# Kernel optimization log

Hardware: AMD Instinct MI355X
Metric: run time of the kernel (lower is better)

Reference implementation:

```python
import jax, jax.numpy as jnp
import numpy as np

N = 100000
IN_F, C1, C2, C3, OUT_F = 64, 64, 64, 64, 8


def setup_inputs() -> dict:
    key = jax.random.key(0)
    ks = jax.random.split(key, 12)
    x = jax.random.normal(ks[0], (N, IN_F), dtype=jnp.float32)
    edge_index = jax.random.randint(ks[1], (2, 1600000), 0, N, dtype=jnp.int64)

    def lin(kw, kb, fi, fo):
        s = 1.0 / np.sqrt(fi)
        W = jax.random.uniform(kw, (fi, fo), jnp.float32, -s, s)
        b = jax.random.uniform(kb, (fo,), jnp.float32, -s, s)
        return W, b

    W1, b1 = lin(ks[2], ks[3], IN_F, C1)
    W2, b2 = lin(ks[4], ks[5], C1, C2)
    W3, b3 = lin(ks[6], ks[7], C2, C3)
    Wl, bl = lin(ks[8], ks[9], C3, OUT_F)
    return {"x": x, "edge_index": edge_index, "W1": W1, "b1": b1,
            "W2": W2, "b2": b2, "W3": W3, "b3": b3, "Wl": Wl, "bl": bl}


def _gcn_norm(edge_index, n):
    # add self loops, compute symmetric normalization D^-1/2 A D^-1/2
    loops = jnp.arange(n, dtype=edge_index.dtype)
    src = jnp.concatenate([edge_index[0], loops])
    dst = jnp.concatenate([edge_index[1], loops])
    deg = jax.ops.segment_sum(jnp.ones_like(dst, dtype=jnp.float32), dst, num_segments=n)
    dis = jnp.where(deg > 0, jax.lax.rsqrt(deg), 0.0)
    norm = dis[src] * dis[dst]  # [E+N]
    return src, dst, norm


def _gcn_layer(h, W, b, src, dst, norm, n):
    h = h @ W                                   # [N, Fout] small GEMM
    msg = h[src] * norm[:, None]                # gather + scale, [E+N, Fout]
    agg = jax.ops.segment_sum(msg, dst, num_segments=n)  # scatter-add
    return agg + b


def reference(x, edge_index, W1, b1, W2, b2, W3, b3, Wl, bl):
    n = x.shape[0]
    src, dst, norm = _gcn_norm(edge_index, n)
    h = jax.nn.relu(_gcn_layer(x, W1, b1, src, dst, norm, n))
    h = jax.nn.relu(_gcn_layer(h, W2, b2, src, dst, norm, n))
    h = jax.nn.relu(_gcn_layer(h, W3, b3, src, dst, norm, n))
    return h @ Wl + bl
```

## Files before the change

### kernel.cpp

```cpp
#include <hip/hip_runtime.h>
#include <hip/hip_fp16.h>

#define F 64
#define CHUNK 2048
#define BN 512
#define BSHIFT 9
#define CAP 20480

typedef int v4i __attribute__((ext_vector_type(4)));
typedef float fx4 __attribute__((ext_vector_type(4)));
typedef float v2f __attribute__((ext_vector_type(2)));
typedef _Float16 h8f __attribute__((ext_vector_type(8)));

union FB8 { uint4 u; h8f h; };
union FX4P { fx4 v; v2f p[2]; };

__global__ __launch_bounds__(256) void k_blkcnt(const int* __restrict__ dst,
                                                int* __restrict__ blkcnt,
                                                int E, int NB, int NBKT) {
    __shared__ int lcnt[256];
    int b = blockIdx.x, t = threadIdx.x;
    lcnt[t] = 0;
    __syncthreads();
    const v4i* d4 = (const v4i*)dst;
    int g0 = (b * CHUNK) >> 2;
    int E4 = E >> 2;
#pragma unroll
    for (int k = 0; k < 2; ++k) {
        int gi = g0 + k * 256 + t;
        if (gi < E4) {
            v4i q = __builtin_nontemporal_load(d4 + gi);
            atomicAdd(&lcnt[q.x >> BSHIFT], 1);
            atomicAdd(&lcnt[q.y >> BSHIFT], 1);
            atomicAdd(&lcnt[q.z >> BSHIFT], 1);
            atomicAdd(&lcnt[q.w >> BSHIFT], 1);
        }
    }
    __syncthreads();
    if (t < NBKT) blkcnt[t * NB + b] = lcnt[t];
}

__global__ __launch_bounds__(256) void k_bktscan(const int* __restrict__ blkcnt,
                                                 int* __restrict__ blkoff,
                                                 int* __restrict__ bkttot, int NB) {
    __shared__ int s[256];
    __shared__ int running;
    int seg = blockIdx.x;
    int t = threadIdx.x;
    if (t == 0) running = 0;
    __syncthreads();
    for (int base = 0; base < NB; base += 256) {
        int i = base + t;
        int v = (i < NB) ? blkcnt[seg * NB + i] : 0;
        s[t] = v;
        __syncthreads();
        for (int off = 1; off < 256; off <<= 1) {
            int x = (t >= off) ? s[t - off] : 0;
            __syncthreads();
            s[t] += x;
            __syncthreads();
        }
        int rbase = running;
        if (i < NB) blkoff[seg * NB + i] = rbase + s[t] - v;
        int ctot = s[255];
        __syncthreads();
        if (t == 0) running = rbase + ctot;
        __syncthreads();
    }
    if (t == 0) bkttot[seg] = running;
}

__global__ void k_sb(const int* __restrict__ bkttot, int* __restrict__ sb, int NBKT) {
    __shared__ int s[256];
    int t = threadIdx.x;
    int v = (t < NBKT) ? bkttot[t] : 0;
    s[t] = v;
    __syncthreads();
    for (int off = 1; off < 256; off <<= 1) {
        int x = (t >= off) ? s[t - off] : 0;
        __syncthreads();
        s[t] += x;
        __syncthreads();
    }
    if (t < NBKT) sb[t] = s[t] - v;
    if (t == NBKT - 1) sb[NBKT] = s[t];
}

__global__ __launch_bounds__(256) void k_stage2(const int* __restrict__ src,
                                                const int* __restrict__ dst,
                                                const int* __restrict__ blkoff,
                                                const int* __restrict__ sb,
                                                unsigned* __restrict__ stage,
                                                int E, int NB, int NBKT) {
    __shared__ int lcnt[256];
    __shared__ int lbase[257];
    __shared__ int obase[256];
    __shared__ int s[256];
    __shared__ unsigned rec[CHUNK];
    __shared__ unsigned char binof[CHUNK];
    int b = blockIdx.x, t = threadIdx.x;
    lcnt[t] = 0;
    __syncthreads();
    const v4i* d4 = (const v4i*)dst;
    const v4i* s4 = (const v4i*)src;
    int g0 = (b * CHUNK) >> 2;
    int E4 = E >> 2;
    int myseg[8], myrank[8];
    unsigned myrec[8];
#pragma unroll
    for (int k = 0; k < 2; ++k) {
        int gi = g0 + k * 256 + t;
        bool ok = gi < E4;
        v4i qd = {0, 0, 0, 0}, qs = {0, 0, 0, 0};
        if (ok) {
            qd = __builtin_nontemporal_load(d4 + gi);
            qs = __builtin_nontemporal_load(s4 + gi);
        }
        int dd[4] = {qd.x, qd.y, qd.z, qd.w};
        int ss[4] = {qs.x, qs.y, qs.z, qs.w};
#pragma unroll
        for (int j = 0; j < 4; ++j) {
            int idx = k * 4 + j;
            myseg[idx] = -1;
            if (ok) {
                int sg = dd[j] >> BSHIFT;
                myseg[idx] = sg;
                myrank[idx] = atomicAdd(&lcnt[sg], 1);
                myrec[idx] = ((unsigned)(dd[j] & (BN - 1)) << 17) | (unsigned)ss[j];
            }
        }
    }
    __syncthreads();
    int v = lcnt[t];
    s[t] = v;
    __syncthreads();
    for (int off = 1; off < 256; off <<= 1) {
        int x = (t >= off) ? s[t - off] : 0;
        __syncthreads();
        s[t] += x;
        __syncthreads();
    }
    lbase[t] = s[t] - v;
    if (t == 255) lbase[256] = s[255];
    obase[t] = (t < NBKT) ? sb[t] + blkoff[t * NB + b] : 0;
    __syncthreads();
#pragma unroll
    for (int k = 0; k < 8; ++k) {
        if (myseg[k] >= 0) {
            int p = lbase[myseg[k]] + myrank[k];
            rec[p] = myrec[k];
            binof[p] = (unsigned char)myseg[k];
        }
    }
    __syncthreads();
    int tot = lbase[256];
    for (int j = t; j < tot; j += 256) {
        int sg = binof[j];
        stage[obase[sg] + (j - lbase[sg])] = rec[j];
    }
}

__global__ __launch_bounds__(1024) void k_bincount(const unsigned* __restrict__ stage,
                                                   const int* __restrict__ sb,
                                                   int* __restrict__ count,
                                                   float* __restrict__ dis,
                                                   int* __restrict__ padtot, int n) {
    __shared__ int lc[BN];
    int bkt = blockIdx.x, t = threadIdx.x;
    int nb0 = bkt << BSHIFT;
    if (t < BN) lc[t] = 0;
    __syncthreads();
    int r0 = sb[bkt], r1 = sb[bkt + 1];
    for (int j = r0 + t; j < r1; j += 1024) {
        unsigned r = stage[j];
        atomicAdd(&lc[r >> 17], 1);
    }
    __syncthreads();
    int pv = 0;
    if (t < BN) {
        int node = nb0 + t;
        int cv = lc[t];
        if (node < n) {
            count[node] = cv;
            dis[node] = rsqrtf((float)(cv + 1));
            pv = (cv + 3) & ~3;
        }
    }
    __syncthreads();
    if (t < BN) lc[t] = pv;
    __syncthreads();
    for (int off = 256; off > 0; off >>= 1) {
        if (t < off) lc[t] += lc[t + off];
        __syncthreads();
    }
    if (t == 0) padtot[bkt] = lc[0];
}

__global__ void k_sb2(const int* __restrict__ padtot, int* __restrict__ rbase,
                      int* __restrict__ row_start, int NBKT, int n) {
    __shared__ int s[256];
    int t = threadIdx.x;
    int v = (t < NBKT) ? padtot[t] : 0;
    s[t] = v;
    __syncthreads();
    for (int off = 1; off < 256; off <<= 1) {
        int x = (t >= off) ? s[t - off] : 0;
        __syncthreads();
        s[t] += x;
        __syncthreads();
    }
    if (t < NBKT) rbase[t] = s[t] - v;
    if (t == NBKT - 1) { rbase[NBKT] = s[t]; row_start[n] = s[t]; }
}

__global__ __launch_bounds__(512) void k_binfill(const unsigned* __restrict__ stage,
                                                 const int* __restrict__ sb,
                                                 const int* __restrict__ count,
                                                 const int* __restrict__ rbase,
                                                 int* __restrict__ row_start,
                                                 int* __restrict__ csr, int n) {
    __shared__ int lcur[BN];
    __shared__ int sc[BN];
    __shared__ int buf[CAP];
    int bkt = blockIdx.x, t = threadIdx.x;
    int nb0 = bkt << BSHIFT;
    int node = nb0 + t;
    int pv = (node < n) ? ((count[node] + 3) & ~3) : 0;
    sc[t] = pv;
    __syncthreads();
    for (int off = 1; off < BN; off <<= 1) {
        int x = (t >= off) ? sc[t - off] : 0;
        __syncthreads();
        sc[t] += x;
        __syncthreads();
    }
    int excl = sc[t] - pv;
    int w0 = rbase[bkt];
    int wlen = sc[BN - 1];
    lcur[t] = excl;
    if (node < n) row_start[node] = w0 + excl;
    for (int j = t; j < wlen && j < CAP; j += 512) buf[j] = n;
    __syncthreads();
    int r0 = sb[bkt], r1 = sb[bkt + 1];
    for (int j = r0 + t; j < r1; j += 512) {
        unsigned r = stage[j];
        int p = atomicAdd(&lcur[r >> 17], 1);
        if (p < CAP) buf[p] = (int)(r & 0x1FFFFu);
    }
    __syncthreads();
    for (int j = t; j < wlen && j < CAP; j += 512) csr[w0 + j] = buf[j];
}

__global__ void k_prep(const float4* __restrict__ x4, const float* __restrict__ dis,
                       uint2* __restrict__ hs, uint2* __restrict__ hs2, int n) {
    int i = blockIdx.x * blockDim.x + threadIdx.x;
    int tot = (n + 1) * 16;
    if (i < tot) {
        int row = i >> 4;
        float dv = 0.0f;
        float4 v = make_float4(0.f, 0.f, 0.f, 0.f);
        if (row < n) { dv = dis[row]; v = x4[i]; }
        __half2 h01 = __floats2half2_rn(dv * v.x, dv * v.y);
        __half2 h23 = __floats2half2_rn(dv * v.z, dv * v.w);
        uint2 u;
        u.x = *(unsigned*)&h01;
        u.y = *(unsigned*)&h23;
        hs[i] = u;
    } else if (i < tot + 16) {
        hs2[(size_t)n * 16 + (i - tot)] = make_uint2(0u, 0u);
    }
}

__global__ __launch_bounds__(512) void k_layer(const __half* __restrict__ hin,
        const float* __restrict__ W, const float* __restrict__ b,
        const int* __restrict__ row_start, const int* __restrict__ csr,
        const float* __restrict__ dis, __half* __restrict__ hout,
        int n, int scale_out) {
    __shared__ char lds_all[32768];
    int tid = threadIdx.x;
    int lane = tid & 63;
    int wv = tid >> 6;
    int r0 = (blockIdx.x * 8 + wv) << 4;
    if (r0 >= n) return;
    char* myLds = lds_all + (wv << 12);
    unsigned short* X16 = (unsigned short*)myLds;
    const uint4* h4 = (const uint4*)hin;

    int r_  = lane & 15;
    int g4  = lane >> 4;
    int q32 = lane >> 1;
    int c2  = lane & 1;

    int lo = row_start[r0 + r_];
    int hi = row_start[r0 + r_ + 1];
    int s0 = __shfl(lo, 0);
    int s4 = __shfl(hi, 15);
    int NBb = (s4 - s0 + 31) >> 5;
    unsigned deg = (unsigned)(hi - lo);

    fx4 acc0 = {0.f, 0.f, 0.f, 0.f};
    fx4 acc1 = acc0, acc2 = acc0, acc3 = acc0;

    auto getnode = [&](int i) -> int {
        if (i < NBb) {
            int slot = s0 + (i << 5) + q32;
            int nd = csr[slot];
            return (slot < s4) ? nd : n;
        }
        return (q32 < 16) ? (r0 + q32) : n;
    };

    int q0 = q32;
    int q1 = q32 ^ 8;
    int q2 = q32 ^ 16;
    int q3 = q32 ^ 24;
    const char* rb = myLds + ((r_ << 6) + ((g4 ^ ((r_ >> 1) & 3)) << 4));

#define PUT1(J, GG) { \
    unsigned short* p = X16 + ((fb + 8 * (J)) << 5); \
    p[q0]       = (unsigned short)(GG.x); \
    p[32 + q0]  = (unsigned short)(GG.x >> 16); \
    p[64 + q1]  = (unsigned short)(GG.y); \
    p[96 + q1]  = (unsigned short)(GG.y >> 16); \
    p[128 + q2] = (unsigned short)(GG.z); \
    p[160 + q2] = (unsigned short)(GG.z >> 16); \
    p[192 + q3] = (unsigned short)(GG.w); \
    p[224 + q3] = (unsigned short)(GG.w >> 16); \
}

#define SMFMA(TT) { \
    unsigned w[4]; \
    if ((TT) < NBb) { \
        unsigned u0 = (unsigned)(s0 + ((TT) << 5) + (g4 << 3)) - (unsigned)lo; \
        w[0] = ((u0     ) < deg ? 0x3C00u : 0u) | ((u0 + 1u) < deg ? 0x3C000000u : 0u); \
        w[1] = ((u0 + 2u) < deg ? 0x3C00u : 0u) | ((u0 + 3u) < deg ? 0x3C000000u : 0u); \
        w[2] = ((u0 + 4u) < deg ? 0x3C00u : 0u) | ((u0 + 5u) < deg ? 0x3C000000u : 0u); \
        w[3] = ((u0 + 6u) < deg ? 0x3C00u : 0u) | ((u0 + 7u) < deg ? 0x3C000000u : 0u); \
    } else { \
        int k0 = g4 << 3; \
        w[0] = ((k0    ) == r_ ? 0x3C00u : 0u) | ((k0 + 1) == r_ ? 0x3C000000u : 0u); \
        w[1] = ((k0 + 2) == r_ ? 0x3C00u : 0u) | ((k0 + 3) == r_ ? 0x3C000000u : 0u); \
        w[2] = ((k0 + 4) == r_ ? 0x3C00u : 0u) | ((k0 + 5) == r_ ? 0x3C000000u : 0u); \
        w[3] = ((k0 + 6) == r_ ? 0x3C00u : 0u) | ((k0 + 7) == r_ ? 0x3C000000u : 0u); \
    } \
    FB8 af; af.u = make_uint4(w[0], w[1], w[2], w[3]); \
    FB8 b0_, b1_, b2_, b3_; \
    b0_.u = *(const uint4*)(rb); \
    b1_.u = *(const uint4*)(rb + 1024); \
    b2_.u = *(const uint4*)(rb + 2048); \
    b3_.u = *(const uint4*)(rb + 3072); \
    acc0 = __builtin_amdgcn_mfma_f32_16x16x32_f16(af.h, b0_.h, acc0, 0, 0, 0); \
    acc1 = __builtin_amdgcn_mfma_f32_16x16x32_f16(af.h, b1_.h, acc1, 0, 0, 0); \
    acc2 = __builtin_amdgcn_mfma_f32_16x16x32_f16(af.h, b2_.h, acc2, 0, 0, 0); \
    acc3 = __builtin_amdgcn_mfma_f32_16x16x32_f16(af.h, b3_.h, acc3, 0, 0, 0); \
}

    uint4 G0, G1, G2, G3, H0, H1, H2, H3;
    int nx;
    {
        int a0 = getnode(0);
        int ba = a0 * 8 + c2 * 4;
        G0 = h4[ba]; G1 = h4[ba + 1]; G2 = h4[ba + 2]; G3 = h4[ba + 3];
        int a1 = getnode(1);
        int bb = a1 * 8 + c2 * 4;
        H0 = h4[bb]; H1 = h4[bb + 1]; H2 = h4[bb + 2]; H3 = h4[bb + 3];
        nx = getnode(2);
    }

    for (int t = 0; ; t += 2) {
        { int fb = c2 << 5; PUT1(0, G0) PUT1(1, G1) PUT1(2, G2) PUT1(3, G3) }
        { int bb = nx * 8 + c2 * 4;
          G0 = h4[bb]; G1 = h4[bb + 1]; G2 = h4[bb + 2]; G3 = h4[bb + 3];
          nx = getnode(t + 3); }
        SMFMA(t)
        if (t + 1 > NBb) break;
        { int fb = c2 << 5; PUT1(0, H0) PUT1(1, H1) PUT1(2, H2) PUT1(3, H3) }
        { int bb = nx * 8 + c2 * 4;
          H0 = h4[bb]; H1 = h4[bb + 1]; H2 = h4[bb + 2]; H3 = h4[bb + 3];
          nx = getnode(t + 4); }
        SMFMA(t + 1)
        if (t + 2 > NBb) break;
    }
#undef PUT1
#undef SMFMA

    float* T = (float*)myLds;
#define TSTORE(S, A) { \
    int fb_ = ((16 * (S) + r_) << 4) + (g4 << 2); \
    *(fx4*)(T + fb_) = A; }
    TSTORE(0, acc0) TSTORE(1, acc1) TSTORE(2, acc2) TSTORE(3, acc3)
#undef TSTORE

    float bb_ = b[lane];
    v2f yv2[8];
#pragma unroll
    for (int k = 0; k < 8; ++k) { yv2[k].x = 0.f; yv2[k].y = 0.f; }
    const float* Wp = W + lane;
#pragma unroll 4
    for (int f = 0; f < 64; ++f) {
        float w = Wp[f << 6];
        v2f wv; wv.x = w; wv.y = w;
        const float* Tf = T + (f << 4);
        FX4P d0, d1, d2, d3;
        d0.v = *(const fx4*)(Tf);
        d1.v = *(const fx4*)(Tf + 4);
        d2.v = *(const fx4*)(Tf + 8);
        d3.v = *(const fx4*)(Tf + 12);
        yv2[0] += d0.p[0] * wv;  yv2[1] += d0.p[1] * wv;
        yv2[2] += d1.p[0] * wv;  yv2[3] += d1.p[1] * wv;
        yv2[4] += d2.p[0] * wv;  yv2[5] += d2.p[1] * wv;
        yv2[6] += d3.p[0] * wv;  yv2[7] += d3.p[1] * wv;
    }

#pragma unroll
    for (int r = 0; r < 16; ++r) {
        float yvr = (r & 1) ? yv2[r >> 1].y : yv2[r >> 1].x;
        float dd = dis[r0 + r];
        float y = fmaxf(yvr * dd + bb_, 0.f);
        if (scale_out) y *= dd;
        hout[((size_t)(r0 + r) << 6) + lane] = __float2half(y);
    }
}

__global__ __launch_bounds__(256) void k_final(const __half* __restrict__ h,
                                               const float* __restrict__ Wl,
                                               const float* __restrict__ bl,
                                               float* __restrict__ out, int n) {
    __shared__ float Ws[F * 8];
    __shared__ float bs[8];
    int tid = threadIdx.x;
    Ws[tid] = Wl[tid];
    Ws[tid + 256] = Wl[tid + 256];
    if (tid < 8) bs[tid] = bl[tid];
    __syncthreads();
    int idx = blockIdx.x * 256 + tid;
    if (idx >= n * 8) return;
    int row = idx >> 3;
    int o = idx & 7;
    const __half* hr = h + (size_t)row * F;
    float acc = bs[o];
#pragma unroll
    for (int k = 0; k < F; ++k) acc = fmaf(__half2float(hr[k]), Ws[k * 8 + o], acc);
    out[idx] = acc;
}

extern "C" void kernel_launch(void* const* d_in, const int* in_sizes, int n_in,
                              void* d_out, int out_size, void* d_ws, size_t ws_size,
                              hipStream_t stream) {
    const float* x  = (const float*)d_in[0];
    const int*   ei = (const int*)d_in[1];
    const float* W1 = (const float*)d_in[2];
    const float* b1 = (const float*)d_in[3];
    const float* W2 = (const float*)d_in[4];
    const float* b2 = (const float*)d_in[5];
    const float* W3 = (const float*)d_in[6];
    const float* b3 = (const float*)d_in[7];
    const float* Wl = (const float*)d_in[8];
    const float* bl = (const float*)d_in[9];
    float* out = (float*)d_out;

    int n = in_sizes[0] / F;
    int E = in_sizes[1] / 2;
    const int* src = ei;
    const int* dst = ei + E;

    int np   = (n + 256) & ~255;
    int cap  = E + 3 * n + 64;
    int NB   = (E + CHUNK - 1) / CHUNK;
    int NBKT = (n + BN - 1) >> BSHIFT;

    int*      count     = (int*)d_ws;
    int*      row_start = count + np;
    int*      blkcnt    = row_start + np;
    int*      blkoff    = blkcnt + 256 * NB;
    int*      bkttot    = blkoff + 256 * NB;
    int*      sb        = bkttot + 256;
    int*      padtot    = sb + 272;
    int*      rbase     = padtot + 256;
    float*    dis       = (float*)(rbase + 272);
    unsigned* stage     = (unsigned*)(dis + np);
    int*      csr       = (int*)(stage + ((E + 3) & ~3));
    __half*   buf1      = (__half*)(csr + ((cap + 3) & ~3));
    __half*   buf2      = buf1 + (size_t)(n + 1) * F;

    k_blkcnt<<<NB, 256, 0, stream>>>(dst, blkcnt, E, NB, NBKT);

    k_bktscan<<<NBKT, 256, 0, stream>>>(blkcnt, blkoff, bkttot, NB);
    k_sb<<<1, 256, 0, stream>>>(bkttot, sb, NBKT);
    k_stage2<<<NB, 256, 0, stream>>>(src, dst, blkoff, sb, stage, E, NB, NBKT);

    k_bincount<<<NBKT, 1024, 0, stream>>>(stage, sb, count, dis, padtot, n);
    k_sb2<<<1, 256, 0, stream>>>(padtot, rbase, row_start, NBKT, n);

    k_binfill<<<NBKT, 512, 0, stream>>>(stage, sb, count, rbase, row_start, csr, n);

    k_prep<<<((n + 1) * 16 + 16 + 255) / 256, 256, 0, stream>>>(
        (const float4*)x, dis, (uint2*)buf1, (uint2*)buf2, n);

    int nb_l = (n + 127) / 128;
    k_layer<<<nb_l, 512, 0, stream>>>(buf1, W1, b1, row_start, csr, dis, buf2, n, 1);
    k_layer<<<nb_l, 512, 0, stream>>>(buf2, W2, b2, row_start, csr, dis, buf1, n, 1);
    k_layer<<<nb_l, 512, 0, stream>>>(buf1, W3, b3, row_start, csr, dis, buf2, n, 0);

    k_final<<<(n * 8 + 255) / 256, 256, 0, stream>>>(buf2, Wl, bl, out, n);
}
```

Measured before the change: 283.4 us.

## Load MFMA B fragments directly from global fp16 rows, drop LDS transpose staging

The aggregation loop used to load whole neighbour rows as uint4 vectors and scatter them into LDS as 16-bit stores to transpose them into MFMA B-operand layout. It now broadcasts neighbour indices with shuffles and has each lane gather individual fp16 elements straight from global memory into the fragment registers, removing the LDS transpose traffic and its stores. The block size also drops from 512 to 256 threads with half the shared memory. The trade-off is many scalar 2-byte global loads per lane instead of wide 16-byte loads, which may raise memory instruction count and hurt coalescing.

```diff
diff --git a/kernel.cpp b/kernel.cpp
--- a/kernel.cpp
+++ b/kernel.cpp
@@ -271,25 +271,23 @@
     }
 }
 
-__global__ __launch_bounds__(512) void k_layer(const __half* __restrict__ hin,
+__global__ __launch_bounds__(256) void k_layer(const __half* __restrict__ hin,
         const float* __restrict__ W, const float* __restrict__ b,
         const int* __restrict__ row_start, const int* __restrict__ csr,
         const float* __restrict__ dis, __half* __restrict__ hout,
         int n, int scale_out) {
-    __shared__ char lds_all[32768];
+    __shared__ char lds_all[16384];
     int tid = threadIdx.x;
     int lane = tid & 63;
     int wv = tid >> 6;
-    int r0 = (blockIdx.x * 8 + wv) << 4;
+    int r0 = (blockIdx.x * 4 + wv) << 4;
     if (r0 >= n) return;
     char* myLds = lds_all + (wv << 12);
-    unsigned short* X16 = (unsigned short*)myLds;
-    const uint4* h4 = (const uint4*)hin;
+    const _Float16* hp = (const _Float16*)hin;
 
     int r_  = lane & 15;
     int g4  = lane >> 4;
-    int q32 = lane >> 1;
-    int c2  = lane & 1;
+    int l31 = lane & 31;
 
     int lo = row_start[r0 + r_];
     int hi = row_start[r0 + r_ + 1];
@@ -301,34 +299,28 @@
     fx4 acc0 = {0.f, 0.f, 0.f, 0.f};
     fx4 acc1 = acc0, acc2 = acc0, acc3 = acc0;
 
-    auto getnode = [&](int i) -> int {
+    auto ldnodes = [&](int i) -> int {
         if (i < NBb) {
-            int slot = s0 + (i << 5) + q32;
+            int slot = s0 + (i << 5) + l31;
             int nd = csr[slot];
             return (slot < s4) ? nd : n;
         }
-        return (q32 < 16) ? (r0 + q32) : n;
+        return (l31 < 16) ? (r0 + l31) : n;
     };
 
-    int q0 = q32;
-    int q1 = q32 ^ 8;
-    int q2 = q32 ^ 16;
-    int q3 = q32 ^ 24;
-    const char* rb = myLds + ((r_ << 6) + ((g4 ^ ((r_ >> 1) & 3)) << 4));
-
-#define PUT1(J, GG) { \
-    unsigned short* p = X16 + ((fb + 8 * (J)) << 5); \
-    p[q0]       = (unsigned short)(GG.x); \
-    p[32 + q0]  = (unsigned short)(GG.x >> 16); \
-    p[64 + q1]  = (unsigned short)(GG.y); \
-    p[96 + q1]  = (unsigned short)(GG.y >> 16); \
-    p[128 + q2] = (unsigned short)(GG.z); \
-    p[160 + q2] = (unsigned short)(GG.z >> 16); \
-    p[192 + q3] = (unsigned short)(GG.w); \
-    p[224 + q3] = (unsigned short)(GG.w >> 16); \
-}
-
-#define SMFMA(TT) { \
+#define LOADFRAG(F0, F1, F2, F3, NDS) { \
+    _Pragma("unroll") \
+    for (int j = 0; j < 8; ++j) { \
+        int ndj = __shfl((NDS), 8 * g4 + j); \
+        const _Float16* rp = hp + (((size_t)(unsigned)ndj) << 6) + r_; \
+        F0.h[j] = rp[0]; \
+        F1.h[j] = rp[16]; \
+        F2.h[j] = rp[32]; \
+        F3.h[j] = rp[48]; \
+    } \
+}
+
+#define SMFMA(TT, F0, F1, F2, F3) { \
     unsigned w[4]; \
     if ((TT) < NBb) { \
         unsigned u0 = (unsigned)(s0 + ((TT) << 5) + (g4 << 3)) - (unsigned)lo; \
@@ -344,44 +336,32 @@
         w[3] = ((k0 + 6) == r_ ? 0x3C00u : 0u) | ((k0 + 7) == r_ ? 0x3C000000u : 0u); \
     } \
     FB8 af; af.u = make_uint4(w[0], w[1], w[2], w[3]); \
-    FB8 b0_, b1_, b2_, b3_; \
-    b0_.u = *(const uint4*)(rb); \
-    b1_.u = *(const uint4*)(rb + 1024); \
-    b2_.u = *(const uint4*)(rb + 2048); \
-    b3_.u = *(const uint4*)(rb + 3072); \
-    acc0 = __builtin_amdgcn_mfma_f32_16x16x32_f16(af.h, b0_.h, acc0, 0, 0, 0); \
-    acc1 = __builtin_amdgcn_mfma_f32_16x16x32_f16(af.h, b1_.h, acc1, 0, 0, 0); \
-    acc2 = __builtin_amdgcn_mfma_f32_16x16x32_f16(af.h, b2_.h, acc2, 0, 0, 0); \
-    acc3 = __builtin_amdgcn_mfma_f32_16x16x32_f16(af.h, b3_.h, acc3, 0, 0, 0); \
-}
-
-    uint4 G0, G1, G2, G3, H0, H1, H2, H3;
-    int nx;
+    acc0 = __builtin_amdgcn_mfma_f32_16x16x32_f16(af.h, F0.h, acc0, 0, 0, 0); \
+    acc1 = __builtin_amdgcn_mfma_f32_16x16x32_f16(af.h, F1.h, acc1, 0, 0, 0); \
+    acc2 = __builtin_amdgcn_mfma_f32_16x16x32_f16(af.h, F2.h, acc2, 0, 0, 0); \
+    acc3 = __builtin_amdgcn_mfma_f32_16x16x32_f16(af.h, F3.h, acc3, 0, 0, 0); \
+}
+
+    FB8 A0, A1, A2, A3, B0, B1, B2, B3;
+    int ndA, ndB;
     {
-        int a0 = getnode(0);
-        int ba = a0 * 8 + c2 * 4;
-        G0 = h4[ba]; G1 = h4[ba + 1]; G2 = h4[ba + 2]; G3 = h4[ba + 3];
-        int a1 = getnode(1);
-        int bb = a1 * 8 + c2 * 4;
-        H0 = h4[bb]; H1 = h4[bb + 1]; H2 = h4[bb + 2]; H3 = h4[bb + 3];
-        nx = getnode(2);
+        int nd0 = ldnodes(0);
+        LOADFRAG(A0, A1, A2, A3, nd0)
+        ndA = ldnodes(1);
+        ndB = ldnodes(2);
     }
 
     for (int t = 0; ; t += 2) {
-        { int fb = c2 << 5; PUT1(0, G0) PUT1(1, G1) PUT1(2, G2) PUT1(3, G3) }
-        { int bb = nx * 8 + c2 * 4;
-          G0 = h4[bb]; G1 = h4[bb + 1]; G2 = h4[bb + 2]; G3 = h4[bb + 3];
-          nx = getnode(t + 3); }
-        SMFMA(t)
+        LOADFRAG(B0, B1, B2, B3, ndA)
+        ndA = ldnodes(t + 3);
+        SMFMA(t, A0, A1, A2, A3)
         if (t + 1 > NBb) break;
-        { int fb = c2 << 5; PUT1(0, H0) PUT1(1, H1) PUT1(2, H2) PUT1(3, H3) }
-        { int bb = nx * 8 + c2 * 4;
-          H0 = h4[bb]; H1 = h4[bb + 1]; H2 = h4[bb + 2]; H3 = h4[bb + 3];
-          nx = getnode(t + 4); }
-        SMFMA(t + 1)
+        LOADFRAG(A0, A1, A2, A3, ndB)
+        ndB = ldnodes(t + 4);
+        SMFMA(t + 1, B0, B1, B2, B3)
         if (t + 2 > NBb) break;
     }
-#undef PUT1
+#undef LOADFRAG
 #undef SMFMA
 
     float* T = (float*)myLds;
@@ -497,10 +477,10 @@
     k_prep<<<((n + 1) * 16 + 16 + 255) / 256, 256, 0, stream>>>(
         (const float4*)x, dis, (uint2*)buf1, (uint2*)buf2, n);
 
-    int nb_l = (n + 127) / 128;
-    k_layer<<<nb_l, 512, 0, stream>>>(buf1, W1, b1, row_start, csr, dis, buf2, n, 1);
-    k_layer<<<nb_l, 512, 0, stream>>>(buf2, W2, b2, row_start, csr, dis, buf1, n, 1);
-    k_layer<<<nb_l, 512, 0, stream>>>(buf1, W3, b3, row_start, csr, dis, buf2, n, 0);
+    int nb_l = (n + 63) / 64;
+    k_layer<<<nb_l, 256, 0, stream>>>(buf1, W1, b1, row_start, csr, dis, buf2, n, 1);
+    k_layer<<<nb_l, 256, 0, stream>>>(buf2, W2, b2, row_start, csr, dis, buf1, n, 1);
+    k_layer<<<nb_l, 256, 0, stream>>>(buf1, W3, b3, row_start, csr, dis, buf2, n, 0);
 
     k_final<<<(n * 8 + 255) / 256, 256, 0, stream>>>(buf2, Wl, bl, out, n);
 }
```

New measurement: 264.8 us. -6.6%, faster.
